# Kernel optimization log

Hardware: AMD Instinct MI355X
Metric: run time of the kernel (lower is better)

The kernel has to match this reference:

```python
import jax, jax.numpy as jnp
import numpy as np

DIM = 1024
HEADS = 16
HEAD_DIM = 64
CHUNK = 128
B = 2
S = 2048  # 2 * N * CHUNK with N = 8


def rotate_half(x):
    # interleaved pair rotation: (x1, x2) -> (-x2, x1)
    x1 = x[..., 0::2]
    x2 = x[..., 1::2]
    return jnp.stack((-x2, x1), axis=-1).reshape(x.shape)


def rms_norm(x, w, eps=1e-6):
    v = jnp.mean(jnp.square(x.astype(jnp.float32)), axis=-1, keepdims=True)
    return (x * jax.lax.rsqrt(v + eps)).astype(x.dtype) * w


def build_chunk_mask(seq_len, chunk_size):
    # Replicates ChunkAttnProcessor training mask (right_mask).
    c = jnp.arange(seq_len) // chunk_size
    ci = c[None, :]   # key-chunk index (columns) -- matches torch's unsqueeze(0)
    cj = c[:, None]   # query-chunk index (rows)  -- matches torch's unsqueeze(1)
    N = seq_len // (2 * chunk_size)  # num_cache_blocks
    max_lookback = 5
    rel_j = cj - N
    mask_self = ci == cj
    mask_cache = (rel_j >= 0) & (ci < N) & (ci < rel_j) & (ci >= rel_j - max_lookback)
    return mask_self | mask_cache  # [S, S] bool, row = query, col = key


def setup_inputs() -> dict:
    key = jax.random.key(0)
    ks = jax.random.split(key, 10)
    x = jax.random.normal(ks[0], (B, S, DIM), jnp.float32)
    mask = jnp.ones((B, S), jnp.bool_)
    # rotary frequency table, interleaved pairs: [S, HEAD_DIM]
    pos = jnp.arange(S, dtype=jnp.float32)
    inv = 1.0 / (10000.0 ** (jnp.arange(0, HEAD_DIM, 2, dtype=jnp.float32) / HEAD_DIM))
    freqs = jnp.repeat(pos[:, None] * inv[None, :], 2, axis=-1)
    inner = HEADS * HEAD_DIM
    sc = 0.02
    Wq = jax.random.normal(ks[1], (inner, DIM), jnp.float32) * sc
    bq = jax.random.normal(ks[2], (inner,), jnp.float32) * sc
    Wk = jax.random.normal(ks[3], (inner, DIM), jnp.float32) * sc
    bk = jax.random.normal(ks[4], (inner,), jnp.float32) * sc
    Wv = jax.random.normal(ks[5], (inner, DIM), jnp.float32) * sc
    bv = jax.random.normal(ks[6], (inner,), jnp.float32) * sc
    Wo = jax.random.normal(ks[7], (DIM, inner), jnp.float32) * sc
    bo = jax.random.normal(ks[8], (DIM,), jnp.float32) * sc
    qw = jnp.ones((HEAD_DIM,), jnp.float32)
    kw = jnp.ones((HEAD_DIM,), jnp.float32)
    return {"x": x, "mask": mask, "freqs": freqs, "Wq": Wq, "bq": bq,
            "Wk": Wk, "bk": bk, "Wv": Wv, "bv": bv, "Wo": Wo, "bo": bo,
            "qw": qw, "kw": kw}


def reference(x, mask, freqs, Wq, bq, Wk, bk, Wv, bv, Wo, bo, qw, kw):
    b, n, _ = x.shape
    # QKV projections (torch Linear: x @ W.T + b)
    q = jnp.einsum('bnd,ed->bne', x, Wq) + bq
    k = jnp.einsum('bnd,ed->bne', x, Wk) + bk
    v = jnp.einsum('bnd,ed->bne', x, Wv) + bv
    q = q.reshape(b, n, HEADS, HEAD_DIM).transpose(0, 2, 1, 3)  # [b,h,n,d]
    k = k.reshape(b, n, HEADS, HEAD_DIM).transpose(0, 2, 1, 3)
    v = v.reshape(b, n, HEADS, HEAD_DIM).transpose(0, 2, 1, 3)
    # qk rms-norm over head_dim
    q = rms_norm(q, qw)
    k = rms_norm(k, kw)
    # rotary embedding (xpos_scale = None -> scale 1.0)
    cos = jnp.cos(freqs)
    sin = jnp.sin(freqs)
    q = q * cos + rotate_half(q) * sin
    k = k * cos + rotate_half(k) * sin
    # block-local + cache-lookback mask (training path), combined with pad mask
    block_mask = build_chunk_mask(n, CHUNK)                                  # [S,S]
    pad = (mask[:, None, :] & mask[:, :, None]) | jnp.eye(n, dtype=bool)[None]
    amask = (block_mask[None] & pad)[:, None]                                # [b,1,S,S]
    # masked SDPA
    scale = 1.0 / np.sqrt(HEAD_DIM)
    logits = jnp.einsum('bhqd,bhkd->bhqk', q, k) * scale
    logits = jnp.where(amask, logits, -jnp.inf)
    attn = jax.nn.softmax(logits, axis=-1)
    o = jnp.einsum('bhqk,bhkd->bhqd', attn, v)
    o = o.transpose(0, 2, 1, 3).reshape(b, n, HEADS * HEAD_DIM)
    o = jnp.einsum('bne,de->bnd', o, Wo) + bo
    o = jnp.where(mask[..., None], o, 0.0)
    return o
```

## Files before the change

kernel.cpp:

```cpp
#include <hip/hip_runtime.h>
#include <stdint.h>
#include <math.h>

typedef unsigned short u16;
typedef __bf16 bf16x8 __attribute__((ext_vector_type(8)));
typedef float f32x4 __attribute__((ext_vector_type(4)));
typedef u16 u16x8 __attribute__((ext_vector_type(8)));

#define DIMD 1024
#define SLEN 2048
#define NHEAD 16
#define HD 64

static __device__ __forceinline__ float b2f(u16 u){ union{float f;uint32_t i;}x; x.i=((uint32_t)u)<<16; return x.f; }
static __device__ __forceinline__ u16 f2b(float f){ union{float f;uint32_t i;}x; x.f=f; uint32_t r=x.i+0x7FFFu+((x.i>>16)&1u); return (u16)(r>>16); }
static __device__ __forceinline__ u16 f2b_fast(float f){ __bf16 h=(__bf16)f; return __builtin_bit_cast(u16,h); }

static __device__ __forceinline__ void gl_lds16(const u16* g, u16* l){
  __builtin_amdgcn_global_load_lds((__attribute__((address_space(1))) void*)g,
                                   (__attribute__((address_space(3))) void*)l, 16, 0, 0);
}
static __device__ __forceinline__ f32x4 mfma16(bf16x8 a, bf16x8 b, f32x4 c){
  return __builtin_amdgcn_mfma_f32_16x16x32_bf16(a, b, c, 0, 0, 0);
}

__global__ __launch_bounds__(256) void k_convert(const float* __restrict__ x,
    const float* __restrict__ wq, const float* __restrict__ wk,
    const float* __restrict__ wv, const float* __restrict__ wo,
    const float* __restrict__ freqs,
    u16* __restrict__ ws, float* __restrict__ cs, float* __restrict__ sn)
{
  const int bid = blockIdx.x;
  if (bid >= 4096){
    const int idx = ((bid-4096)*256 + threadIdx.x)*8;
    #pragma unroll
    for (int j=0;j<8;++j){
      float c, s;
      __sincosf(freqs[idx+j], &s, &c);
      cs[idx+j]=c; sn[idx+j]=s;
    }
    return;
  }
  const float* src; u16* dst; int idx;
  if (bid < 2048){ src=x; dst=ws; idx=(bid*256+threadIdx.x)*8; }
  else {
    const int t = (bid-2048)>>9, blk = (bid-2048)&511;
    src = (t==0)?wq:((t==1)?wk:((t==2)?wv:wo));
    dst = ws + ((size_t)(4+t)<<20);
    idx = (blk*256+threadIdx.x)*8;
  }
  const float4* s4 = (const float4*)(src+idx);
  float4 a = s4[0], b = s4[1];
  u16x8 r;
  r[0]=f2b(a.x); r[1]=f2b(a.y); r[2]=f2b(a.z); r[3]=f2b(a.w);
  r[4]=f2b(b.x); r[5]=f2b(b.y); r[6]=f2b(b.z); r[7]=f2b(b.w);
  *(u16x8*)(dst+idx) = r;
}

__global__ __launch_bounds__(256,3) void k_gemm_qkv(const u16* __restrict__ A,
    const u16* __restrict__ wq, const u16* __restrict__ wk, const u16* __restrict__ wv,
    const float* __restrict__ bq, const float* __restrict__ bk, const float* __restrict__ bv,
    const float* __restrict__ cs_t, const float* __restrict__ sn_t,
    const float* __restrict__ qw, const float* __restrict__ kw,
    u16* __restrict__ qo, u16* __restrict__ ko, u16* __restrict__ vo)
{
  __shared__ u16 Al[128*64];
  __shared__ u16 Bl[128*64];
  const int tid = threadIdx.x, lane = tid&63, w = tid>>6;
  const int L15 = lane&15, g = lane>>4;
  const int mb = blockIdx.x;
  const int yy = blockIdx.y;
  const int t = yy>>3, nb = yy&7;
  const u16* Bm = (t==0)?wq:((t==1)?wk:wv);
  const float* bias = (t==0)?bq:((t==1)?bk:bv);
  u16* dst = (t==0)?qo:((t==1)?ko:vo);
  const int wm=(w&1)*64, wn=(w>>1)*64;
  f32x4 acc[4][4];
  #pragma unroll
  for(int i=0;i<4;++i){
    #pragma unroll
    for(int j=0;j<4;++j) acc[i][j]=0;
  }
  const u16* Ab = A  + (size_t)mb*128*DIMD;
  const u16* Bb = Bm + (size_t)nb*128*DIMD;
  const int srow8 = lane>>3;
  const int kxor  = ((lane&7) ^ srow8)*8;
  for (int kt=0; kt<16; ++kt){
    const int kk = kt*64;
    #pragma unroll
    for (int c2=0;c2<4;++c2){
      const int c = w*4+c2;
      const int row = c*8 + srow8;
      gl_lds16(Ab + row*DIMD + kk + kxor, Al + c*512);
      gl_lds16(Bb + row*DIMD + kk + kxor, Bl + c*512);
    }
    __syncthreads();
    bf16x8 af[4][2], bf[4][2];
    #pragma unroll
    for (int mt=0;mt<4;++mt){
      const int row = wm+mt*16+L15;
      #pragma unroll
      for (int ks=0;ks<2;++ks)
        af[mt][ks]=*(const bf16x8*)(Al + row*64 + 8*((ks*4+g) ^ (row&7)));
    }
    #pragma unroll
    for (int nt=0;nt<4;++nt){
      const int row = wn+nt*16+L15;
      #pragma unroll
      for (int ks=0;ks<2;++ks)
        bf[nt][ks]=*(const bf16x8*)(Bl + row*64 + 8*((ks*4+g) ^ (row&7)));
    }
    #pragma unroll
    for (int mt=0;mt<4;++mt){
      #pragma unroll
      for (int nt=0;nt<4;++nt){
        acc[mt][nt]=mfma16(af[mt][0], bf[nt][0], acc[mt][nt]);
        acc[mt][nt]=mfma16(af[mt][1], bf[nt][1], acc[mt][nt]);
      }
    }
    __syncthreads();
  }
  float bias_v[4];
  #pragma unroll
  for (int nt=0;nt<4;++nt) bias_v[nt] = bias[nb*128 + wn + nt*16 + L15];

  if (t < 2){
    const float* wt = (t==0)? qw : kw;
    const float scale = (t==0)? 0.125f*1.44269504089f : 1.0f;
    const int h = (nb*128 + wn) >> 6;
    float wt_v[4];
    #pragma unroll
    for (int nt=0;nt<4;++nt) wt_v[nt] = wt[nt*16 + L15];
    #pragma unroll
    for (int mt=0;mt<4;++mt){
      #pragma unroll
      for (int r=0;r<4;++r){
        float val[4]; float ss=0.f;
        #pragma unroll
        for (int nt=0;nt<4;++nt){ val[nt]=acc[mt][nt][r]+bias_v[nt]; ss+=val[nt]*val[nt]; }
        #pragma unroll
        for (int sh=1; sh<16; sh<<=1) ss += __shfl_xor(ss, sh);
        const float rin = rsqrtf(ss*(1.0f/HD) + 1e-6f);
        const int rowM = mb*128 + wm + mt*16 + g*4 + r;
        const int b2 = rowM>>11, s = rowM&(SLEN-1);
        const size_t rb = ((size_t)((b2*NHEAD+h)*SLEN+s))*HD;
        #pragma unroll
        for (int nt=0;nt<4;++nt){
          const int d = nt*16 + L15;
          float xn = val[nt]*rin*wt_v[nt];
          float cv = cs_t[s*HD + d], sv = sn_t[s*HD + d];
          float pa = __shfl_xor(xn, 1);
          float rot = (L15&1) ? pa : -pa;
          dst[rb + d] = f2b((xn*cv + rot*sv)*scale);
        }
      }
    }
  } else {
    #pragma unroll
    for (int nt=0;nt<4;++nt){
      const int c = nb*128 + wn + nt*16 + L15;
      const int h = c>>6, d = c&63;
      #pragma unroll
      for (int mt=0;mt<4;++mt){
        #pragma unroll
        for (int r=0;r<4;++r){
          const int rowM = mb*128 + wm + mt*16 + g*4 + r;
          const int b2 = rowM>>11, s = rowM&(SLEN-1);
          dst[((size_t)((b2*NHEAD+h)*SLEN+s))*HD + d] = f2b(acc[mt][nt][r]+bias_v[nt]);
        }
      }
    }
  }
}

__global__ __launch_bounds__(256,3) void k_gemm_out(const u16* __restrict__ A,
    const u16* __restrict__ Bm, const float* __restrict__ bias, float* __restrict__ out)
{
  __shared__ u16 Al[128*64];
  __shared__ u16 Bl[64*64];
  const int tid = threadIdx.x, lane = tid&63, w = tid>>6;
  const int L15 = lane&15, g = lane>>4;
  const int mb = blockIdx.x;
  const int nb = blockIdx.y;
  const int wm=(w&1)*64, wn=(w>>1)*32;
  f32x4 acc[4][2];
  #pragma unroll
  for(int i=0;i<4;++i){
    #pragma unroll
    for(int j=0;j<2;++j) acc[i][j]=0;
  }
  const u16* Ab = A  + (size_t)mb*128*DIMD;
  const u16* Bb = Bm + (size_t)nb*64*DIMD;
  const int srow8 = lane>>3;
  const int kxor  = ((lane&7) ^ srow8)*8;
  for (int kt=0; kt<16; ++kt){
    const int kk = kt*64;
    #pragma unroll
    for (int c2=0;c2<4;++c2){
      const int c = w*4+c2;
      const int row = c*8 + srow8;
      gl_lds16(Ab + row*DIMD + kk + kxor, Al + c*512);
    }
    #pragma unroll
    for (int c2=0;c2<2;++c2){
      const int c = w*2+c2;
      const int row = c*8 + srow8;
      gl_lds16(Bb + row*DIMD + kk + kxor, Bl + c*512);
    }
    __syncthreads();
    bf16x8 af[4][2], bf[2][2];
    #pragma unroll
    for (int mt=0;mt<4;++mt){
      const int row = wm+mt*16+L15;
      #pragma unroll
      for (int ks=0;ks<2;++ks)
        af[mt][ks]=*(const bf16x8*)(Al + row*64 + 8*((ks*4+g) ^ (row&7)));
    }
    #pragma unroll
    for (int nt=0;nt<2;++nt){
      const int row = wn+nt*16+L15;
      #pragma unroll
      for (int ks=0;ks<2;++ks)
        bf[nt][ks]=*(const bf16x8*)(Bl + row*64 + 8*((ks*4+g) ^ (row&7)));
    }
    #pragma unroll
    for (int mt=0;mt<4;++mt){
      #pragma unroll
      for (int nt=0;nt<2;++nt){
        acc[mt][nt]=mfma16(af[mt][0], bf[nt][0], acc[mt][nt]);
        acc[mt][nt]=mfma16(af[mt][1], bf[nt][1], acc[mt][nt]);
      }
    }
    __syncthreads();
  }
  #pragma unroll
  for (int nt=0;nt<2;++nt){
    const int c = nb*64 + wn + nt*16 + L15;
    const float bv_ = bias[c];
    #pragma unroll
    for (int mt=0;mt<4;++mt){
      #pragma unroll
      for (int r=0;r<4;++r){
        const int rowM = mb*128 + wm + mt*16 + g*4 + r;
        out[(size_t)rowM*DIMD + c] = acc[mt][nt][r]+bv_;
      }
    }
  }
}

__global__ __launch_bounds__(256,2) void k_attn(const u16* __restrict__ qb, const u16* __restrict__ kb,
    const u16* __restrict__ vb, u16* __restrict__ ob)
{
  __shared__ u16 VT[64*128];
  __shared__ u16 Kl[128*64];
  __shared__ u16 Pl[4*32*136];
  __shared__ float Lb[4][32];
  const int tid=threadIdx.x, lane=tid&63, w=tid>>6;
  const int L15=lane&15, g=lane>>4;
  const int q3=L15&7;
  const int bid=blockIdx.x;
  const int b_=bid>>8;
  const int t2=bid&255;
  const int h=(t2>>4)&15;
  const int c0=t2&15;
  const int qc = b_ ? (15-c0) : c0;
  const size_t bh=(size_t)(b_*NHEAD+h);
  const u16* qp = qb + (bh*SLEN + qc*128)*HD;

  bf16x8 qf[2][2];
  #pragma unroll
  for (int qt=0;qt<2;++qt){
    #pragma unroll
    for (int ks=0;ks<2;++ks)
      qf[qt][ks]=*(const bf16x8*)(qp + (w*32+qt*16+L15)*HD + ks*32 + g*8);
  }

  f32x4 accO[2][4];
  float ps[2]={0.f,0.f};
  #pragma unroll
  for (int qt=0;qt<2;++qt){
    #pragma unroll
    for(int dt=0;dt<4;++dt) accO[qt][dt]=0;
  }

  int kcs[6]; int nk=0; kcs[nk++]=qc;
  if (qc>=9){
    int lo=qc-13; if(lo<0)lo=0;
    const int hi=qc-9;
    for(int kc=lo;kc<=hi;++kc) kcs[nk++]=kc;
  }
  u16* Pw = Pl + w*32*136;

  const int krow = tid>>3, kk8 = tid&7;
  const int vk0 = (tid&31)*2, vdc = (tid>>5)*8;
  u16x8 kreg[4], vreg0[2], vreg1[2];
  {
    const u16* kp = kb + (bh*SLEN + kcs[0]*128)*HD;
    const u16* vp = vb + (bh*SLEN + kcs[0]*128)*HD;
    #pragma unroll
    for (int i=0;i<4;++i) kreg[i]=*(const u16x8*)(kp + (krow+i*32)*HD + kk8*8);
    #pragma unroll
    for (int p=0;p<2;++p){
      vreg0[p]=*(const u16x8*)(vp + (p*64+vk0  )*HD + vdc);
      vreg1[p]=*(const u16x8*)(vp + (p*64+vk0+1)*HD + vdc);
    }
  }

  for (int it=0; it<nk; ++it){
    #pragma unroll
    for (int i=0;i<4;++i){
      const int row = krow+i*32;
      *(u16x8*)(Kl + row*HD + 8*(kk8 ^ (row&7))) = kreg[i];
    }
    #pragma unroll
    for (int p=0;p<2;++p){
      const int k0 = p*64 + vk0;
      #pragma unroll
      for (int j=0;j<8;++j){
        const int d = vdc+j;
        const int kx = k0 ^ ((d&7)<<3);
        *(uint32_t*)(VT + d*128 + kx) = (uint32_t)vreg0[p][j] | ((uint32_t)vreg1[p][j]<<16);
      }
    }
    __syncthreads();
    if (it+1 < nk){
      const int kc2 = kcs[it+1];
      const u16* kp = kb + (bh*SLEN + kc2*128)*HD;
      const u16* vp = vb + (bh*SLEN + kc2*128)*HD;
      #pragma unroll
      for (int i=0;i<4;++i) kreg[i]=*(const u16x8*)(kp + (krow+i*32)*HD + kk8*8);
      #pragma unroll
      for (int p=0;p<2;++p){
        vreg0[p]=*(const u16x8*)(vp + (p*64+vk0  )*HD + vdc);
        vreg1[p]=*(const u16x8*)(vp + (p*64+vk0+1)*HD + vdc);
      }
    }
    #pragma unroll
    for (int kt2=0;kt2<8;++kt2){
      const int row = kt2*16+L15;
      const u16* kr = Kl + row*HD;
      bf16x8 kf0 = *(const bf16x8*)(kr + 8*((g  ) ^ (row&7)));
      bf16x8 kf1 = *(const bf16x8*)(kr + 8*((g+4) ^ (row&7)));
      f32x4 st[2];
      #pragma unroll
      for (int qt=0;qt<2;++qt){
        f32x4 cc=0;
        cc=mfma16(kf0, qf[qt][0], cc);
        cc=mfma16(kf1, qf[qt][1], cc);
        st[qt]=cc;
      }
      #pragma unroll
      for (int qt=0;qt<2;++qt){
        float x0=exp2f(st[qt][0]), x1=exp2f(st[qt][1]);
        float x2=exp2f(st[qt][2]), x3=exp2f(st[qt][3]);
        ps[qt] += (x0+x1)+(x2+x3);
        uint2 pk;
        pk.x = (uint32_t)f2b_fast(x0) | ((uint32_t)f2b_fast(x1)<<16);
        pk.y = (uint32_t)f2b_fast(x2) | ((uint32_t)f2b_fast(x3)<<16);
        *(uint2*)(Pw + (qt*16+L15)*136 + ((kt2 ^ q3)*16 + g*4)) = pk;
      }
    }
    const int g1=g>>1, g0=g&1;
    #pragma unroll
    for (int ks=0;ks<4;++ks){
      bf16x8 pf[2], vf[4];
      #pragma unroll
      for (int qt=0;qt<2;++qt)
        pf[qt]=*(const bf16x8*)(Pw + (qt*16+L15)*136 + (((ks*2+g1) ^ q3)*16 + g0*8));
      #pragma unroll
      for (int dt=0;dt<4;++dt){
        const int n=dt*16+L15;
        vf[dt]=*(const bf16x8*)(VT + n*128 + ((ks*32+g*8) ^ ((n&7)<<3)));
      }
      #pragma unroll
      for (int qt=0;qt<2;++qt){
        #pragma unroll
        for (int dt=0;dt<4;++dt)
          accO[qt][dt]=mfma16(pf[qt],vf[dt],accO[qt][dt]);
      }
    }
    __syncthreads();
  }

  #pragma unroll
  for (int qt=0;qt<2;++qt){
    float l=ps[qt];
    l += __shfl_xor(l,16);
    l += __shfl_xor(l,32);
    if (g==0) Lb[w][qt*16+L15]=l;
  }
  #pragma unroll
  for (int qt=0;qt<2;++qt){
    #pragma unroll
    for (int r=0;r<4;++r){
      const float inv=1.0f/Lb[w][qt*16+g*4+r];
      const int srow=qc*128 + w*32 + qt*16 + g*4 + r;
      #pragma unroll
      for (int dt=0;dt<4;++dt){
        const size_t di=((size_t)(b_*SLEN+srow))*DIMD + h*HD + dt*16 + L15;
        ob[di]=f2b_fast(accO[qt][dt][r]*inv);
      }
    }
  }
}

extern "C" void kernel_launch(void* const* d_in, const int* in_sizes, int n_in,
                              void* d_out, int out_size, void* d_ws, size_t ws_size,
                              hipStream_t stream)
{
  (void)in_sizes; (void)n_in; (void)out_size; (void)ws_size;
  const float* x     = (const float*)d_in[0];
  const float* freqs = (const float*)d_in[2];
  const float* Wq    = (const float*)d_in[3];
  const float* bq    = (const float*)d_in[4];
  const float* Wk    = (const float*)d_in[5];
  const float* bk    = (const float*)d_in[6];
  const float* Wv    = (const float*)d_in[7];
  const float* bv    = (const float*)d_in[8];
  const float* Wo    = (const float*)d_in[9];
  const float* bo    = (const float*)d_in[10];
  const float* qw    = (const float*)d_in[11];
  const float* kw    = (const float*)d_in[12];

  u16* ws  = (u16*)d_ws;
  u16* xb  = ws;
  u16* wqb = ws + (4u<<20);
  u16* wkb = ws + (5u<<20);
  u16* wvb = ws + (6u<<20);
  u16* wob = ws + (7u<<20);
  u16* q   = ws + (8u<<20);
  u16* k   = ws + (12u<<20);
  u16* v   = ws + (16u<<20);
  u16* o   = ws + (20u<<20);
  float* cs = (float*)(ws + (24u<<20));
  float* sn = cs + SLEN*HD;

  k_convert<<<4160,256,0,stream>>>(x,Wq,Wk,Wv,Wo,freqs,ws,cs,sn);
  k_gemm_qkv<<<dim3(32,24),256,0,stream>>>(xb,wqb,wkb,wvb,bq,bk,bv,cs,sn,qw,kw,q,k,v);
  k_attn<<<512,256,0,stream>>>(q,k,v,o);
  k_gemm_out<<<dim3(32,16),256,0,stream>>>(o,wob,bo,(float*)d_out);
}
```

Measured before the change: 165.5 us.

## Compute Q and K tiles in one block to share A loads; interleave rotary table

The QKV GEMM now has each block in the first half of the grid compute both the Q and K output tiles from one shared A tile, with two B buffers in LDS. V is computed by a separate set of blocks, which shrinks the grid from 24 to 16 in y and halves A traffic for Q/K. The cos/sin tables are interleaved into one float2 array so the epilogue issues one load instead of two. Manual bf16 rounding is replaced with the hardware cast, and the attention Q load is moved after the K/V prefetch. The doubled accumulators lower occupancy (launch bounds 3 to 2) and leave the V blocks with half the work of the Q/K blocks, so load is imbalanced.

```diff
diff --git a/kernel.cpp b/kernel.cpp
--- a/kernel.cpp
+++ b/kernel.cpp
@@ -12,8 +12,6 @@
 #define NHEAD 16
 #define HD 64
 
-static __device__ __forceinline__ float b2f(u16 u){ union{float f;uint32_t i;}x; x.i=((uint32_t)u)<<16; return x.f; }
-static __device__ __forceinline__ u16 f2b(float f){ union{float f;uint32_t i;}x; x.f=f; uint32_t r=x.i+0x7FFFu+((x.i>>16)&1u); return (u16)(r>>16); }
 static __device__ __forceinline__ u16 f2b_fast(float f){ __bf16 h=(__bf16)f; return __builtin_bit_cast(u16,h); }
 
 static __device__ __forceinline__ void gl_lds16(const u16* g, u16* l){
@@ -28,7 +26,7 @@
     const float* __restrict__ wq, const float* __restrict__ wk,
     const float* __restrict__ wv, const float* __restrict__ wo,
     const float* __restrict__ freqs,
-    u16* __restrict__ ws, float* __restrict__ cs, float* __restrict__ sn)
+    u16* __restrict__ ws, float2* __restrict__ tab)
 {
   const int bid = blockIdx.x;
   if (bid >= 4096){
@@ -37,7 +35,7 @@
     for (int j=0;j<8;++j){
       float c, s;
       __sincosf(freqs[idx+j], &s, &c);
-      cs[idx+j]=c; sn[idx+j]=s;
+      tab[idx+j] = make_float2(c, s);
     }
     return;
   }
@@ -52,37 +50,40 @@
   const float4* s4 = (const float4*)(src+idx);
   float4 a = s4[0], b = s4[1];
   u16x8 r;
-  r[0]=f2b(a.x); r[1]=f2b(a.y); r[2]=f2b(a.z); r[3]=f2b(a.w);
-  r[4]=f2b(b.x); r[5]=f2b(b.y); r[6]=f2b(b.z); r[7]=f2b(b.w);
+  r[0]=f2b_fast(a.x); r[1]=f2b_fast(a.y); r[2]=f2b_fast(a.z); r[3]=f2b_fast(a.w);
+  r[4]=f2b_fast(b.x); r[5]=f2b_fast(b.y); r[6]=f2b_fast(b.z); r[7]=f2b_fast(b.w);
   *(u16x8*)(dst+idx) = r;
 }
 
-__global__ __launch_bounds__(256,3) void k_gemm_qkv(const u16* __restrict__ A,
+__global__ __launch_bounds__(256,2) void k_gemm_qkv(const u16* __restrict__ A,
     const u16* __restrict__ wq, const u16* __restrict__ wk, const u16* __restrict__ wv,
     const float* __restrict__ bq, const float* __restrict__ bk, const float* __restrict__ bv,
-    const float* __restrict__ cs_t, const float* __restrict__ sn_t,
+    const float2* __restrict__ tab,
     const float* __restrict__ qw, const float* __restrict__ kw,
     u16* __restrict__ qo, u16* __restrict__ ko, u16* __restrict__ vo)
 {
   __shared__ u16 Al[128*64];
-  __shared__ u16 Bl[128*64];
+  __shared__ u16 Bl[2][128*64];
   const int tid = threadIdx.x, lane = tid&63, w = tid>>6;
   const int L15 = lane&15, g = lane>>4;
   const int mb = blockIdx.x;
   const int yy = blockIdx.y;
-  const int t = yy>>3, nb = yy&7;
-  const u16* Bm = (t==0)?wq:((t==1)?wk:wv);
-  const float* bias = (t==0)?bq:((t==1)?bk:bv);
-  u16* dst = (t==0)?qo:((t==1)?ko:vo);
+  const bool isqk = yy < 8;
+  const int nb = isqk ? yy : (yy-8);
+  const int NT = isqk ? 2 : 1;
+  const u16* B0 = isqk ? wq : wv;
+  const u16* B1 = wk;
   const int wm=(w&1)*64, wn=(w>>1)*64;
-  f32x4 acc[4][4];
-  #pragma unroll
-  for(int i=0;i<4;++i){
-    #pragma unroll
-    for(int j=0;j<4;++j) acc[i][j]=0;
-  }
-  const u16* Ab = A  + (size_t)mb*128*DIMD;
-  const u16* Bb = Bm + (size_t)nb*128*DIMD;
+  f32x4 acc[2][4][4];
+  #pragma unroll
+  for(int t=0;t<2;++t)
+    #pragma unroll
+    for(int i=0;i<4;++i)
+      #pragma unroll
+      for(int j=0;j<4;++j) acc[t][i][j]=0;
+  const u16* Ab  = A  + (size_t)mb*128*DIMD;
+  const u16* Bb0 = B0 + (size_t)nb*128*DIMD;
+  const u16* Bb1 = B1 + (size_t)nb*128*DIMD;
   const int srow8 = lane>>3;
   const int kxor  = ((lane&7) ^ srow8)*8;
   for (int kt=0; kt<16; ++kt){
@@ -91,11 +92,19 @@
     for (int c2=0;c2<4;++c2){
       const int c = w*4+c2;
       const int row = c*8 + srow8;
-      gl_lds16(Ab + row*DIMD + kk + kxor, Al + c*512);
-      gl_lds16(Bb + row*DIMD + kk + kxor, Bl + c*512);
-    }
-    __syncthreads();
-    bf16x8 af[4][2], bf[4][2];
+      gl_lds16(Ab  + row*DIMD + kk + kxor, Al    + c*512);
+      gl_lds16(Bb0 + row*DIMD + kk + kxor, Bl[0] + c*512);
+    }
+    if (isqk){
+      #pragma unroll
+      for (int c2=0;c2<4;++c2){
+        const int c = w*4+c2;
+        const int row = c*8 + srow8;
+        gl_lds16(Bb1 + row*DIMD + kk + kxor, Bl[1] + c*512);
+      }
+    }
+    __syncthreads();
+    bf16x8 af[4][2];
     #pragma unroll
     for (int mt=0;mt<4;++mt){
       const int row = wm+mt*16+L15;
@@ -103,55 +112,61 @@
       for (int ks=0;ks<2;++ks)
         af[mt][ks]=*(const bf16x8*)(Al + row*64 + 8*((ks*4+g) ^ (row&7)));
     }
-    #pragma unroll
-    for (int nt=0;nt<4;++nt){
-      const int row = wn+nt*16+L15;
-      #pragma unroll
-      for (int ks=0;ks<2;++ks)
-        bf[nt][ks]=*(const bf16x8*)(Bl + row*64 + 8*((ks*4+g) ^ (row&7)));
-    }
-    #pragma unroll
-    for (int mt=0;mt<4;++mt){
+    for (int t=0;t<NT;++t){
+      bf16x8 bf[4][2];
       #pragma unroll
       for (int nt=0;nt<4;++nt){
-        acc[mt][nt]=mfma16(af[mt][0], bf[nt][0], acc[mt][nt]);
-        acc[mt][nt]=mfma16(af[mt][1], bf[nt][1], acc[mt][nt]);
-      }
-    }
-    __syncthreads();
-  }
-  float bias_v[4];
-  #pragma unroll
-  for (int nt=0;nt<4;++nt) bias_v[nt] = bias[nb*128 + wn + nt*16 + L15];
-
-  if (t < 2){
-    const float* wt = (t==0)? qw : kw;
-    const float scale = (t==0)? 0.125f*1.44269504089f : 1.0f;
-    const int h = (nb*128 + wn) >> 6;
-    float wt_v[4];
-    #pragma unroll
-    for (int nt=0;nt<4;++nt) wt_v[nt] = wt[nt*16 + L15];
-    #pragma unroll
-    for (int mt=0;mt<4;++mt){
-      #pragma unroll
-      for (int r=0;r<4;++r){
-        float val[4]; float ss=0.f;
+        const int row = wn+nt*16+L15;
         #pragma unroll
-        for (int nt=0;nt<4;++nt){ val[nt]=acc[mt][nt][r]+bias_v[nt]; ss+=val[nt]*val[nt]; }
-        #pragma unroll
-        for (int sh=1; sh<16; sh<<=1) ss += __shfl_xor(ss, sh);
-        const float rin = rsqrtf(ss*(1.0f/HD) + 1e-6f);
-        const int rowM = mb*128 + wm + mt*16 + g*4 + r;
-        const int b2 = rowM>>11, s = rowM&(SLEN-1);
-        const size_t rb = ((size_t)((b2*NHEAD+h)*SLEN+s))*HD;
+        for (int ks=0;ks<2;++ks)
+          bf[nt][ks]=*(const bf16x8*)(Bl[t] + row*64 + 8*((ks*4+g) ^ (row&7)));
+      }
+      #pragma unroll
+      for (int mt=0;mt<4;++mt){
         #pragma unroll
         for (int nt=0;nt<4;++nt){
-          const int d = nt*16 + L15;
-          float xn = val[nt]*rin*wt_v[nt];
-          float cv = cs_t[s*HD + d], sv = sn_t[s*HD + d];
-          float pa = __shfl_xor(xn, 1);
-          float rot = (L15&1) ? pa : -pa;
-          dst[rb + d] = f2b((xn*cv + rot*sv)*scale);
+          acc[t][mt][nt]=mfma16(af[mt][0], bf[nt][0], acc[t][mt][nt]);
+          acc[t][mt][nt]=mfma16(af[mt][1], bf[nt][1], acc[t][mt][nt]);
+        }
+      }
+    }
+    __syncthreads();
+  }
+  if (isqk){
+    const int h = (nb*128 + wn) >> 6;
+    for (int t=0;t<2;++t){
+      const float* bias = t ? bk : bq;
+      const float* wt   = t ? kw : qw;
+      u16* dst          = t ? ko : qo;
+      const float scale = t ? 1.0f : 0.125f*1.44269504089f;
+      float bias_v[4], wt_v[4];
+      #pragma unroll
+      for (int nt=0;nt<4;++nt){
+        bias_v[nt] = bias[nb*128 + wn + nt*16 + L15];
+        wt_v[nt]   = wt[nt*16 + L15];
+      }
+      #pragma unroll
+      for (int mt=0;mt<4;++mt){
+        #pragma unroll
+        for (int r=0;r<4;++r){
+          float val[4]; float ss=0.f;
+          #pragma unroll
+          for (int nt=0;nt<4;++nt){ val[nt]=acc[t][mt][nt][r]+bias_v[nt]; ss+=val[nt]*val[nt]; }
+          #pragma unroll
+          for (int sh=1; sh<16; sh<<=1) ss += __shfl_xor(ss, sh);
+          const float rin = rsqrtf(ss*(1.0f/HD) + 1e-6f);
+          const int rowM = mb*128 + wm + mt*16 + g*4 + r;
+          const int b2 = rowM>>11, s = rowM&(SLEN-1);
+          const size_t rb = ((size_t)((b2*NHEAD+h)*SLEN+s))*HD;
+          #pragma unroll
+          for (int nt=0;nt<4;++nt){
+            const int d = nt*16 + L15;
+            float xn = val[nt]*rin*wt_v[nt];
+            float2 cssn = tab[s*HD + d];
+            float pa = __shfl_xor(xn, 1);
+            float rot = (L15&1) ? pa : -pa;
+            dst[rb + d] = f2b_fast((xn*cssn.x + rot*cssn.y)*scale);
+          }
         }
       }
     }
@@ -159,6 +174,7 @@
     #pragma unroll
     for (int nt=0;nt<4;++nt){
       const int c = nb*128 + wn + nt*16 + L15;
+      const float bv_ = bv[c];
       const int h = c>>6, d = c&63;
       #pragma unroll
       for (int mt=0;mt<4;++mt){
@@ -166,7 +182,7 @@
         for (int r=0;r<4;++r){
           const int rowM = mb*128 + wm + mt*16 + g*4 + r;
           const int b2 = rowM>>11, s = rowM&(SLEN-1);
-          dst[((size_t)((b2*NHEAD+h)*SLEN+s))*HD + d] = f2b(acc[mt][nt][r]+bias_v[nt]);
+          vo[((size_t)((b2*NHEAD+h)*SLEN+s))*HD + d] = f2b_fast(acc[0][mt][nt][r]+bv_);
         }
       }
     }
@@ -267,29 +283,12 @@
   const size_t bh=(size_t)(b_*NHEAD+h);
   const u16* qp = qb + (bh*SLEN + qc*128)*HD;
 
-  bf16x8 qf[2][2];
-  #pragma unroll
-  for (int qt=0;qt<2;++qt){
-    #pragma unroll
-    for (int ks=0;ks<2;++ks)
-      qf[qt][ks]=*(const bf16x8*)(qp + (w*32+qt*16+L15)*HD + ks*32 + g*8);
-  }
-
-  f32x4 accO[2][4];
-  float ps[2]={0.f,0.f};
-  #pragma unroll
-  for (int qt=0;qt<2;++qt){
-    #pragma unroll
-    for(int dt=0;dt<4;++dt) accO[qt][dt]=0;
-  }
-
   int kcs[6]; int nk=0; kcs[nk++]=qc;
   if (qc>=9){
     int lo=qc-13; if(lo<0)lo=0;
     const int hi=qc-9;
     for(int kc=lo;kc<=hi;++kc) kcs[nk++]=kc;
   }
-  u16* Pw = Pl + w*32*136;
 
   const int krow = tid>>3, kk8 = tid&7;
   const int vk0 = (tid&31)*2, vdc = (tid>>5)*8;
@@ -305,6 +304,23 @@
       vreg1[p]=*(const u16x8*)(vp + (p*64+vk0+1)*HD + vdc);
     }
   }
+
+  bf16x8 qf[2][2];
+  #pragma unroll
+  for (int qt=0;qt<2;++qt){
+    #pragma unroll
+    for (int ks=0;ks<2;++ks)
+      qf[qt][ks]=*(const bf16x8*)(qp + (w*32+qt*16+L15)*HD + ks*32 + g*8);
+  }
+
+  f32x4 accO[2][4];
+  float ps[2]={0.f,0.f};
+  #pragma unroll
+  for (int qt=0;qt<2;++qt){
+    #pragma unroll
+    for(int dt=0;dt<4;++dt) accO[qt][dt]=0;
+  }
+  u16* Pw = Pl + w*32*136;
 
   for (int it=0; it<nk; ++it){
     #pragma unroll
@@ -432,11 +448,10 @@
   u16* k   = ws + (12u<<20);
   u16* v   = ws + (16u<<20);
   u16* o   = ws + (20u<<20);
-  float* cs = (float*)(ws + (24u<<20));
-  float* sn = cs + SLEN*HD;
-
-  k_convert<<<4160,256,0,stream>>>(x,Wq,Wk,Wv,Wo,freqs,ws,cs,sn);
-  k_gemm_qkv<<<dim3(32,24),256,0,stream>>>(xb,wqb,wkb,wvb,bq,bk,bv,cs,sn,qw,kw,q,k,v);
+  float2* tab = (float2*)(ws + (24u<<20));
+
+  k_convert<<<4160,256,0,stream>>>(x,Wq,Wk,Wv,Wo,freqs,ws,tab);
+  k_gemm_qkv<<<dim3(32,16),256,0,stream>>>(xb,wqb,wkb,wvb,bq,bk,bv,tab,qw,kw,q,k,v);
   k_attn<<<512,256,0,stream>>>(q,k,v,o);
   k_gemm_out<<<dim3(32,16),256,0,stream>>>(o,wob,bo,(float*)d_out);
 }
```

After: 176.9 us. +6.9%, slower.

## Register-prefetch GEMM tiles instead of direct global-to-LDS loads

Applied to the files above, without the earlier changes.

Both projection GEMM kernels drop the global_load_lds path. They now prefetch the next K-tile into registers while the current tile is computed, then write it to LDS after a barrier, with the barrier pair moved to the top of the loop. The aim is to hide global load latency behind MFMA work within a single LDS buffer, at the cost of extra registers and explicit LDS store instructions. The attention kernel also reorders its Q fragment loads and accumulator init to after the K/V prefetch issue.

```diff
diff --git a/kernel.cpp b/kernel.cpp
--- a/kernel.cpp
+++ b/kernel.cpp
@@ -16,10 +16,6 @@
 static __device__ __forceinline__ u16 f2b(float f){ union{float f;uint32_t i;}x; x.f=f; uint32_t r=x.i+0x7FFFu+((x.i>>16)&1u); return (u16)(r>>16); }
 static __device__ __forceinline__ u16 f2b_fast(float f){ __bf16 h=(__bf16)f; return __builtin_bit_cast(u16,h); }
 
-static __device__ __forceinline__ void gl_lds16(const u16* g, u16* l){
-  __builtin_amdgcn_global_load_lds((__attribute__((address_space(1))) void*)g,
-                                   (__attribute__((address_space(3))) void*)l, 16, 0, 0);
-}
 static __device__ __forceinline__ f32x4 mfma16(bf16x8 a, bf16x8 b, f32x4 c){
   return __builtin_amdgcn_mfma_f32_16x16x32_bf16(a, b, c, 0, 0, 0);
 }
@@ -85,16 +81,31 @@
   const u16* Bb = Bm + (size_t)nb*128*DIMD;
   const int srow8 = lane>>3;
   const int kxor  = ((lane&7) ^ srow8)*8;
+  u16x8 aP[4], bP[4];
+  #pragma unroll
+  for (int c2=0;c2<4;++c2){
+    const int row = (w*4+c2)*8 + srow8;
+    aP[c2] = *(const u16x8*)(Ab + row*DIMD + kxor);
+    bP[c2] = *(const u16x8*)(Bb + row*DIMD + kxor);
+  }
   for (int kt=0; kt<16; ++kt){
-    const int kk = kt*64;
+    __syncthreads();
     #pragma unroll
     for (int c2=0;c2<4;++c2){
       const int c = w*4+c2;
-      const int row = c*8 + srow8;
-      gl_lds16(Ab + row*DIMD + kk + kxor, Al + c*512);
-      gl_lds16(Bb + row*DIMD + kk + kxor, Bl + c*512);
-    }
-    __syncthreads();
+      *(u16x8*)(Al + c*512 + lane*8) = aP[c2];
+      *(u16x8*)(Bl + c*512 + lane*8) = bP[c2];
+    }
+    __syncthreads();
+    if (kt+1 < 16){
+      const int kk = (kt+1)*64;
+      #pragma unroll
+      for (int c2=0;c2<4;++c2){
+        const int row = (w*4+c2)*8 + srow8;
+        aP[c2] = *(const u16x8*)(Ab + row*DIMD + kk + kxor);
+        bP[c2] = *(const u16x8*)(Bb + row*DIMD + kk + kxor);
+      }
+    }
     bf16x8 af[4][2], bf[4][2];
     #pragma unroll
     for (int mt=0;mt<4;++mt){
@@ -118,7 +129,6 @@
         acc[mt][nt]=mfma16(af[mt][1], bf[nt][1], acc[mt][nt]);
       }
     }
-    __syncthreads();
   }
   float bias_v[4];
   #pragma unroll
@@ -193,21 +203,43 @@
   const u16* Bb = Bm + (size_t)nb*64*DIMD;
   const int srow8 = lane>>3;
   const int kxor  = ((lane&7) ^ srow8)*8;
+  u16x8 aP[4], bP[2];
+  #pragma unroll
+  for (int c2=0;c2<4;++c2){
+    const int row = (w*4+c2)*8 + srow8;
+    aP[c2] = *(const u16x8*)(Ab + row*DIMD + kxor);
+  }
+  #pragma unroll
+  for (int c2=0;c2<2;++c2){
+    const int row = (w*2+c2)*8 + srow8;
+    bP[c2] = *(const u16x8*)(Bb + row*DIMD + kxor);
+  }
   for (int kt=0; kt<16; ++kt){
-    const int kk = kt*64;
+    __syncthreads();
     #pragma unroll
     for (int c2=0;c2<4;++c2){
       const int c = w*4+c2;
-      const int row = c*8 + srow8;
-      gl_lds16(Ab + row*DIMD + kk + kxor, Al + c*512);
+      *(u16x8*)(Al + c*512 + lane*8) = aP[c2];
     }
     #pragma unroll
     for (int c2=0;c2<2;++c2){
       const int c = w*2+c2;
-      const int row = c*8 + srow8;
-      gl_lds16(Bb + row*DIMD + kk + kxor, Bl + c*512);
-    }
-    __syncthreads();
+      *(u16x8*)(Bl + c*512 + lane*8) = bP[c2];
+    }
+    __syncthreads();
+    if (kt+1 < 16){
+      const int kk = (kt+1)*64;
+      #pragma unroll
+      for (int c2=0;c2<4;++c2){
+        const int row = (w*4+c2)*8 + srow8;
+        aP[c2] = *(const u16x8*)(Ab + row*DIMD + kk + kxor);
+      }
+      #pragma unroll
+      for (int c2=0;c2<2;++c2){
+        const int row = (w*2+c2)*8 + srow8;
+        bP[c2] = *(const u16x8*)(Bb + row*DIMD + kk + kxor);
+      }
+    }
     bf16x8 af[4][2], bf[2][2];
     #pragma unroll
     for (int mt=0;mt<4;++mt){
@@ -231,7 +263,6 @@
         acc[mt][nt]=mfma16(af[mt][1], bf[nt][1], acc[mt][nt]);
       }
     }
-    __syncthreads();
   }
   #pragma unroll
   for (int nt=0;nt<2;++nt){
@@ -267,29 +298,12 @@
   const size_t bh=(size_t)(b_*NHEAD+h);
   const u16* qp = qb + (bh*SLEN + qc*128)*HD;
 
-  bf16x8 qf[2][2];
-  #pragma unroll
-  for (int qt=0;qt<2;++qt){
-    #pragma unroll
-    for (int ks=0;ks<2;++ks)
-      qf[qt][ks]=*(const bf16x8*)(qp + (w*32+qt*16+L15)*HD + ks*32 + g*8);
-  }
-
-  f32x4 accO[2][4];
-  float ps[2]={0.f,0.f};
-  #pragma unroll
-  for (int qt=0;qt<2;++qt){
-    #pragma unroll
-    for(int dt=0;dt<4;++dt) accO[qt][dt]=0;
-  }
-
   int kcs[6]; int nk=0; kcs[nk++]=qc;
   if (qc>=9){
     int lo=qc-13; if(lo<0)lo=0;
     const int hi=qc-9;
     for(int kc=lo;kc<=hi;++kc) kcs[nk++]=kc;
   }
-  u16* Pw = Pl + w*32*136;
 
   const int krow = tid>>3, kk8 = tid&7;
   const int vk0 = (tid&31)*2, vdc = (tid>>5)*8;
@@ -305,6 +319,23 @@
       vreg1[p]=*(const u16x8*)(vp + (p*64+vk0+1)*HD + vdc);
     }
   }
+
+  bf16x8 qf[2][2];
+  #pragma unroll
+  for (int qt=0;qt<2;++qt){
+    #pragma unroll
+    for (int ks=0;ks<2;++ks)
+      qf[qt][ks]=*(const bf16x8*)(qp + (w*32+qt*16+L15)*HD + ks*32 + g*8);
+  }
+
+  f32x4 accO[2][4];
+  float ps[2]={0.f,0.f};
+  #pragma unroll
+  for (int qt=0;qt<2;++qt){
+    #pragma unroll
+    for(int dt=0;dt<4;++dt) accO[qt][dt]=0;
+  }
+  u16* Pw = Pl + w*32*136;
 
   for (int it=0; it<nk; ++it){
     #pragma unroll
```

Measured after the change: 170.5 us. +3.1%, slower.
